# Kernel tuning notes

Hardware: AMD Instinct MI355X
Metric: run time of the kernel (lower is better)

## Reference

```python
import jax, jax.numpy as jnp
import numpy as np

BITS = 8
EPS = 1e-08
D_IN = 4096
D_OUT = 4096


def setup_inputs() -> dict:
    key = jax.random.key(0)
    k1, k2, k3 = jax.random.split(key, 3)
    hidden_states = jax.random.normal(k1, (4, 2048, D_IN), dtype=jnp.float32)
    # Pre-quantized (dequantized-value) weight buffer, as the module stores it in float
    qmax = 2 ** (BITS - 1) - 1
    w = jax.random.normal(k2, (D_IN, D_OUT), dtype=jnp.float32) * 0.02
    w_scale = jnp.max(jnp.abs(w)) / qmax
    weight_quantized = jnp.clip(jnp.round(w / w_scale), -qmax, qmax) * w_scale
    bias = jax.random.normal(k3, (D_OUT,), dtype=jnp.float32) * 0.01
    x_scale = jnp.asarray(3.0, dtype=jnp.float32)  # calibrated activation maxabs
    return {
        "hidden_states": hidden_states,
        "weight_quantized": weight_quantized,
        "x_scale": x_scale,
        "bias": bias,
    }


def _quantize_maxabs(x, scale, bits, eps):
    # scalar max-abs quantization with a fixed (calibrated) scale
    qmax = 2 ** (bits - 1) - 1
    step = jnp.maximum(scale, eps) / qmax
    return jnp.clip(jnp.round(x / step), -qmax, qmax) * step


def reference(hidden_states, weight_quantized, x_scale, bias):
    orig_shape = hidden_states.shape[:-1]
    d = hidden_states.shape[-1]
    x_flat = hidden_states.reshape(-1, d)
    x_q = _quantize_maxabs(x_flat, x_scale, BITS, EPS).astype(weight_quantized.dtype)
    out = x_q @ weight_quantized  # [tokens, d_out]
    out = out + bias.astype(out.dtype)[None, :]
    out = out.astype(hidden_states.dtype)
    return out.reshape(*orig_shape, weight_quantized.shape[1])
```

## Files before the change

kernel.cpp:

```cpp
#include <hip/hip_runtime.h>
#include <hip/hip_bf16.h>
#include <cstdint>

#define D_IN  4096
#define D_OUT 4096

typedef __attribute__((ext_vector_type(4))) int   i32x4;
typedef __attribute__((ext_vector_type(4))) float f32x4;

typedef const __attribute__((address_space(1))) unsigned g_u32;
typedef __attribute__((address_space(3))) unsigned       l_u32;

__global__ void wmax1_kernel(const float* __restrict__ W,
                             float* __restrict__ bmax, int n) {
    __shared__ float red[256];
    int tid = threadIdx.x;
    float m = 0.f;
    for (int i = (blockIdx.x * 256 + tid) * 4; i < n; i += gridDim.x * 256 * 4) {
        float4 v = *(const float4*)(W + i);
        m = fmaxf(m, fmaxf(fmaxf(fabsf(v.x), fabsf(v.y)),
                           fmaxf(fabsf(v.z), fabsf(v.w))));
    }
    red[tid] = m; __syncthreads();
    for (int s = 128; s > 0; s >>= 1) {
        if (tid < s) red[tid] = fmaxf(red[tid], red[tid + s]);
        __syncthreads();
    }
    if (tid == 0) bmax[blockIdx.x] = red[0];
}

__global__ void wmax2_kernel(const float* __restrict__ bmax,
                             float* __restrict__ ws) {
    __shared__ float red[1024];
    int tid = threadIdx.x;
    red[tid] = bmax[tid]; __syncthreads();
    for (int s = 512; s > 0; s >>= 1) {
        if (tid < s) red[tid] = fmaxf(red[tid], red[tid + s]);
        __syncthreads();
    }
    if (tid == 0) ws[0] = red[0] * (1.0f / 127.0f);
}

__global__ void quant_x_kernel(const float* __restrict__ x,
                               char* __restrict__ xq,
                               const float* __restrict__ xscale, int n) {
    int i = (blockIdx.x * blockDim.x + threadIdx.x) * 4;
    if (i >= n) return;
    float inv = 127.0f / fmaxf(xscale[0], 1e-8f);
    float4 v = *(const float4*)(x + i);
    char4 o;
    o.x = (char)fminf(fmaxf(rintf(v.x * inv), -127.f), 127.f);
    o.y = (char)fminf(fmaxf(rintf(v.y * inv), -127.f), 127.f);
    o.z = (char)fminf(fmaxf(rintf(v.z * inv), -127.f), 127.f);
    o.w = (char)fminf(fmaxf(rintf(v.w * inv), -127.f), 127.f);
    *(char4*)(xq + i) = o;
}

__global__ void convW_kernel(const float* __restrict__ W,
                             char* __restrict__ Wt,
                             const float* __restrict__ ws) {
    __shared__ float tile[32][33];
    float invws = 1.0f / ws[0];
    int n0 = blockIdx.x * 32, k0 = blockIdx.y * 32;
    tile[threadIdx.y][threadIdx.x] =
        W[(size_t)(k0 + threadIdx.y) * D_OUT + n0 + threadIdx.x];
    __syncthreads();
    Wt[(size_t)(n0 + threadIdx.y) * D_IN + k0 + threadIdx.x] =
        (char)rintf(tile[threadIdx.x][threadIdx.y] * invws);
}

__global__ __launch_bounds__(512, 2)
void gemm_kernel(const char* __restrict__ A,
                 const char* __restrict__ Bt,
                 const float* __restrict__ bias,
                 const float* __restrict__ xscale,
                 const float* __restrict__ wsp,
                 float* __restrict__ C, int M) {
    constexpr int K = D_IN, N = D_OUT;
    constexpr int NT = K / 128;
    __shared__ char lds[2 * 65536];

    const int tid  = threadIdx.x;
    const int lane = tid & 63;
    const int wid  = tid >> 6;
    const int wr   = wid >> 2;
    const int wc   = wid & 3;

    const int nTn = N / 256;
    const int nwg = gridDim.x;
    int bid = blockIdx.x;
    int q8 = nwg >> 3, r8 = nwg & 7;
    int xcd = bid & 7, idx = bid >> 3;
    int swz = (xcd < r8 ? xcd * (q8 + 1) : r8 * (q8 + 1) + (xcd - r8) * q8) + idx;
    const int tm = swz / nTn, tn = swz % nTn;
    const int row0 = tm * 256, col0 = tn * 256;

    int srcOff[4], dstOff[4];
#pragma unroll
    for (int i = 0; i < 4; ++i) {
        int p  = (i * 512 + tid) * 16;
        int sw = p ^ (((p >> 7) & 7) << 4);
        dstOff[i] = p;
        srcOff[i] = (sw >> 7) * K + (sw & 127);
    }

    const char* srcA = A  + (size_t)row0 * K;
    const char* srcB = Bt + (size_t)col0 * K;
    char* ldsb = lds;

    auto STAGE4 = [&](const char* src, char* dst) {
#pragma unroll
        for (int i = 0; i < 4; ++i)
            __builtin_amdgcn_global_load_lds((g_u32*)(src + srcOff[i]),
                                             (l_u32*)(dst + dstOff[i]), 16, 0, 0);
    };
    auto STAGE2 = [&](const char* src, char* dst) {
#pragma unroll
        for (int i = 0; i < 2; ++i)
            __builtin_amdgcn_global_load_lds((g_u32*)(src + srcOff[i]),
                                             (l_u32*)(dst + dstOff[i]), 16, 0, 0);
    };

    STAGE2(srcB, ldsb + 32768);
    STAGE4(srcA, ldsb);
    STAGE2(srcB + 128 * K, ldsb + 32768 + 16384);
    STAGE2(srcB + 128,     ldsb + 65536 + 32768);
    STAGE4(srcA + 128,     ldsb + 65536);

    i32x4 acc[8][4];
#pragma unroll
    for (int m = 0; m < 8; ++m)
#pragma unroll
        for (int n = 0; n < 4; ++n) acc[m][n] = (i32x4){0, 0, 0, 0};

    const int cp0 = (((lane >> 4) << 4)) ^ ((lane & 7) << 4);
    const int cp1 = cp0 ^ 64;
    const int aBase = (wr * 128 + (lane & 15)) * 128;
    const int bBase = (wc * 64  + (lane & 15)) * 128;

    asm volatile("s_waitcnt vmcnt(6)" ::: "memory");

    auto KITER = [&](int t, char* cur, char* nxt) {
        i32x4 a[4][2], b01[2][2], b23[2][2];
        const char* cA = cur;
        const char* cB = cur + 32768;

        __builtin_amdgcn_s_barrier();
        if (t + 1 < NT) STAGE2(srcB + 128 * K + (t + 1) * 128, nxt + 32768 + 16384);

#pragma unroll
        for (int n = 0; n < 2; ++n) {
            b01[n][0] = *(const i32x4*)(cB + bBase + n * 2048 + cp0);
            b01[n][1] = *(const i32x4*)(cB + bBase + n * 2048 + cp1);
        }
#pragma unroll
        for (int m = 0; m < 4; ++m) {
            a[m][0] = *(const i32x4*)(cA + aBase + m * 2048 + cp0);
            a[m][1] = *(const i32x4*)(cA + aBase + m * 2048 + cp1);
        }
#pragma unroll
        for (int n = 0; n < 2; ++n) {
            b23[n][0] = *(const i32x4*)(cB + bBase + 4096 + n * 2048 + cp0);
            b23[n][1] = *(const i32x4*)(cB + bBase + 4096 + n * 2048 + cp1);
        }

        __builtin_amdgcn_s_setprio(1);
#pragma unroll
        for (int m = 0; m < 4; ++m)
#pragma unroll
            for (int n = 0; n < 2; ++n) {
                acc[m][n] = __builtin_amdgcn_mfma_i32_16x16x64_i8(a[m][0], b01[n][0], acc[m][n], 0, 0, 0);
                acc[m][n] = __builtin_amdgcn_mfma_i32_16x16x64_i8(a[m][1], b01[n][1], acc[m][n], 0, 0, 0);
            }
#pragma unroll
        for (int m = 0; m < 4; ++m)
#pragma unroll
            for (int n = 0; n < 2; ++n) {
                acc[m][n + 2] = __builtin_amdgcn_mfma_i32_16x16x64_i8(a[m][0], b23[n][0], acc[m][n + 2], 0, 0, 0);
                acc[m][n + 2] = __builtin_amdgcn_mfma_i32_16x16x64_i8(a[m][1], b23[n][1], acc[m][n + 2], 0, 0, 0);
            }
#pragma unroll
        for (int m = 0; m < 4; ++m) {
            a[m][0] = *(const i32x4*)(cA + aBase + 8192 + m * 2048 + cp0);
            a[m][1] = *(const i32x4*)(cA + aBase + 8192 + m * 2048 + cp1);
        }
#pragma unroll
        for (int m = 0; m < 4; ++m)
#pragma unroll
            for (int n = 0; n < 2; ++n) {
                acc[m + 4][n + 2] = __builtin_amdgcn_mfma_i32_16x16x64_i8(a[m][0], b23[n][0], acc[m + 4][n + 2], 0, 0, 0);
                acc[m + 4][n + 2] = __builtin_amdgcn_mfma_i32_16x16x64_i8(a[m][1], b23[n][1], acc[m + 4][n + 2], 0, 0, 0);
            }
#pragma unroll
        for (int m = 0; m < 4; ++m)
#pragma unroll
            for (int n = 0; n < 2; ++n) {
                acc[m + 4][n] = __builtin_amdgcn_mfma_i32_16x16x64_i8(a[m][0], b01[n][0], acc[m + 4][n], 0, 0, 0);
                acc[m + 4][n] = __builtin_amdgcn_mfma_i32_16x16x64_i8(a[m][1], b01[n][1], acc[m + 4][n], 0, 0, 0);
            }
        __builtin_amdgcn_s_setprio(0);

        __builtin_amdgcn_s_barrier();
        if (t + 2 < NT) {
            STAGE2(srcB + (t + 2) * 128, cur + 32768);
            STAGE4(srcA + (t + 2) * 128, cur);
            asm volatile("s_waitcnt vmcnt(6)" ::: "memory");
        } else {
            asm volatile("s_waitcnt vmcnt(0)" ::: "memory");
        }
    };

    for (int t = 0; t < NT; t += 2) {
        KITER(t,     ldsb,         ldsb + 65536);
        KITER(t + 1, ldsb + 65536, ldsb);
    }

    const float scale = (fmaxf(xscale[0], 1e-8f) * (1.0f / 127.0f)) * wsp[0];
    const int lr = (lane >> 4) * 4, lc = lane & 15;
#pragma unroll
    for (int n = 0; n < 4; ++n) {
        int col = col0 + wc * 64 + n * 16 + lc;
        float bv = bias[col];
#pragma unroll
        for (int m = 0; m < 8; ++m) {
            int rowb = row0 + wr * 128 + m * 16 + lr;
            i32x4 v = acc[m][n];
#pragma unroll
            for (int r2 = 0; r2 < 4; ++r2)
                C[(size_t)(rowb + r2) * N + col] = (float)v[r2] * scale + bv;
        }
    }
}

extern "C" void kernel_launch(void* const* d_in, const int* in_sizes, int n_in,
                              void* d_out, int out_size, void* d_ws, size_t ws_size,
                              hipStream_t stream) {
    const float* x      = (const float*)d_in[0];
    const float* W      = (const float*)d_in[1];
    const float* xscale = (const float*)d_in[2];
    const float* bias   = (const float*)d_in[3];
    float* out = (float*)d_out;

    const int nx = in_sizes[0];
    const int nw = in_sizes[1];
    const int M  = nx / D_IN;

    char*  xq   = (char*)d_ws;
    char*  Wt   = (char*)d_ws + (size_t)nx;
    float* bmax = (float*)((char*)d_ws + (size_t)nx + nw);
    float* wsp  = bmax + 1024;

    wmax1_kernel<<<1024, 256, 0, stream>>>(W, bmax, nw);
    wmax2_kernel<<<1, 1024, 0, stream>>>(bmax, wsp);

    quant_x_kernel<<<nx / 4 / 256, 256, 0, stream>>>(x, xq, xscale, nx);

    dim3 tb(32, 32);
    dim3 tg(D_OUT / 32, D_IN / 32);
    convW_kernel<<<tg, tb, 0, stream>>>(W, Wt, wsp);

    int grid = (M / 256) * (D_OUT / 256);
    gemm_kernel<<<grid, 512, 0, stream>>>(xq, Wt, bias, xscale, wsp, out, M);
}
```

Baseline: 209.9 us.

## Fuse prep kernels and switch GEMM to 32x32x32 int8 MFMA tiles

Merges the weight max-reduction stage 1 and activation quantization into one launch, and folds the final weight-scale reduction into every convW block, which drops two launches. The GEMM inner loop moves from 16x16x64 to 32x32x32 int8 MFMA with 16-wide accumulators and new swizzled LDS offsets, and the epilogue is rewritten for the 32x32 output layout. In exchange, each of the 16K convW blocks now repeats a 1024-element reduction, and the larger MFMA shape changes register pressure and LDS read patterns.

```diff
diff --git a/kernel.cpp b/kernel.cpp
--- a/kernel.cpp
+++ b/kernel.cpp
@@ -5,62 +5,63 @@
 #define D_IN  4096
 #define D_OUT 4096
 
-typedef __attribute__((ext_vector_type(4))) int   i32x4;
-typedef __attribute__((ext_vector_type(4))) float f32x4;
+typedef __attribute__((ext_vector_type(4)))  int   i32x4;
+typedef __attribute__((ext_vector_type(16))) int   i32x16;
 
 typedef const __attribute__((address_space(1))) unsigned g_u32;
 typedef __attribute__((address_space(3))) unsigned       l_u32;
 
-__global__ void wmax1_kernel(const float* __restrict__ W,
-                             float* __restrict__ bmax, int n) {
-    __shared__ float red[256];
+__global__ void prep_kernel(const float* __restrict__ W, int nw,
+                            const float* __restrict__ x,
+                            char* __restrict__ xq,
+                            const float* __restrict__ xscale, int nx,
+                            float* __restrict__ bmax) {
     int tid = threadIdx.x;
-    float m = 0.f;
-    for (int i = (blockIdx.x * 256 + tid) * 4; i < n; i += gridDim.x * 256 * 4) {
-        float4 v = *(const float4*)(W + i);
-        m = fmaxf(m, fmaxf(fmaxf(fabsf(v.x), fabsf(v.y)),
-                           fmaxf(fabsf(v.z), fabsf(v.w))));
-    }
-    red[tid] = m; __syncthreads();
-    for (int s = 128; s > 0; s >>= 1) {
-        if (tid < s) red[tid] = fmaxf(red[tid], red[tid + s]);
-        __syncthreads();
-    }
-    if (tid == 0) bmax[blockIdx.x] = red[0];
-}
-
-__global__ void wmax2_kernel(const float* __restrict__ bmax,
-                             float* __restrict__ ws) {
-    __shared__ float red[1024];
-    int tid = threadIdx.x;
-    red[tid] = bmax[tid]; __syncthreads();
-    for (int s = 512; s > 0; s >>= 1) {
-        if (tid < s) red[tid] = fmaxf(red[tid], red[tid + s]);
-        __syncthreads();
-    }
-    if (tid == 0) ws[0] = red[0] * (1.0f / 127.0f);
-}
-
-__global__ void quant_x_kernel(const float* __restrict__ x,
-                               char* __restrict__ xq,
-                               const float* __restrict__ xscale, int n) {
-    int i = (blockIdx.x * blockDim.x + threadIdx.x) * 4;
-    if (i >= n) return;
-    float inv = 127.0f / fmaxf(xscale[0], 1e-8f);
-    float4 v = *(const float4*)(x + i);
-    char4 o;
-    o.x = (char)fminf(fmaxf(rintf(v.x * inv), -127.f), 127.f);
-    o.y = (char)fminf(fmaxf(rintf(v.y * inv), -127.f), 127.f);
-    o.z = (char)fminf(fmaxf(rintf(v.z * inv), -127.f), 127.f);
-    o.w = (char)fminf(fmaxf(rintf(v.w * inv), -127.f), 127.f);
-    *(char4*)(xq + i) = o;
+    if (blockIdx.x < 1024) {
+        __shared__ float red[256];
+        float m = 0.f;
+        for (int i = (blockIdx.x * 256 + tid) * 4; i < nw; i += 1024 * 256 * 4) {
+            float4 v = *(const float4*)(W + i);
+            m = fmaxf(m, fmaxf(fmaxf(fabsf(v.x), fabsf(v.y)),
+                               fmaxf(fabsf(v.z), fabsf(v.w))));
+        }
+        red[tid] = m; __syncthreads();
+        for (int s = 128; s > 0; s >>= 1) {
+            if (tid < s) red[tid] = fmaxf(red[tid], red[tid + s]);
+            __syncthreads();
+        }
+        if (tid == 0) bmax[blockIdx.x] = red[0];
+    } else {
+        int i = ((blockIdx.x - 1024) * 256 + tid) * 4;
+        if (i >= nx) return;
+        float inv = 127.0f / fmaxf(xscale[0], 1e-8f);
+        float4 v = *(const float4*)(x + i);
+        char4 o;
+        o.x = (char)fminf(fmaxf(rintf(v.x * inv), -127.f), 127.f);
+        o.y = (char)fminf(fmaxf(rintf(v.y * inv), -127.f), 127.f);
+        o.z = (char)fminf(fmaxf(rintf(v.z * inv), -127.f), 127.f);
+        o.w = (char)fminf(fmaxf(rintf(v.w * inv), -127.f), 127.f);
+        *(char4*)(xq + i) = o;
+    }
 }
 
 __global__ void convW_kernel(const float* __restrict__ W,
                              char* __restrict__ Wt,
-                             const float* __restrict__ ws) {
+                             const float* __restrict__ bmax,
+                             float* __restrict__ wsp) {
     __shared__ float tile[32][33];
-    float invws = 1.0f / ws[0];
+    __shared__ float red[1024];
+    int lt = threadIdx.y * 32 + threadIdx.x;
+    red[lt] = bmax[lt]; __syncthreads();
+    for (int s = 512; s > 0; s >>= 1) {
+        if (lt < s) red[lt] = fmaxf(red[lt], red[lt + s]);
+        __syncthreads();
+    }
+    float wmax = red[0];
+    float invws = 127.0f / wmax;
+    if (lt == 0 && blockIdx.x == 0 && blockIdx.y == 0)
+        wsp[0] = wmax * (1.0f / 127.0f);
+
     int n0 = blockIdx.x * 32, k0 = blockIdx.y * 32;
     tile[threadIdx.y][threadIdx.x] =
         W[(size_t)(k0 + threadIdx.y) * D_OUT + n0 + threadIdx.x];
@@ -127,21 +128,26 @@
     STAGE2(srcB + 128,     ldsb + 65536 + 32768);
     STAGE4(srcA + 128,     ldsb + 65536);
 
-    i32x4 acc[8][4];
-#pragma unroll
-    for (int m = 0; m < 8; ++m)
-#pragma unroll
-        for (int n = 0; n < 4; ++n) acc[m][n] = (i32x4){0, 0, 0, 0};
-
-    const int cp0 = (((lane >> 4) << 4)) ^ ((lane & 7) << 4);
-    const int cp1 = cp0 ^ 64;
-    const int aBase = (wr * 128 + (lane & 15)) * 128;
-    const int bBase = (wc * 64  + (lane & 15)) * 128;
+    i32x16 acc[4][2];
+#pragma unroll
+    for (int m = 0; m < 4; ++m)
+#pragma unroll
+        for (int n = 0; n < 2; ++n)
+#pragma unroll
+            for (int r = 0; r < 16; ++r) acc[m][n][r] = 0;
+
+    const int sw7 = (lane & 7) << 4;
+    const int hi16 = (lane >> 5) * 16;
+    int coff[4];
+#pragma unroll
+    for (int ks = 0; ks < 4; ++ks) coff[ks] = (ks * 32 + hi16) ^ sw7;
+    const int aRow = (wr * 128 + (lane & 31)) * 128;
+    const int bRow = (wc * 64  + (lane & 31)) * 128;
 
     asm volatile("s_waitcnt vmcnt(6)" ::: "memory");
 
     auto KITER = [&](int t, char* cur, char* nxt) {
-        i32x4 a[4][2], b01[2][2], b23[2][2];
+        i32x4 a[4][2], b[2][2];
         const char* cA = cur;
         const char* cB = cur + 32768;
 
@@ -150,53 +156,41 @@
 
 #pragma unroll
         for (int n = 0; n < 2; ++n) {
-            b01[n][0] = *(const i32x4*)(cB + bBase + n * 2048 + cp0);
-            b01[n][1] = *(const i32x4*)(cB + bBase + n * 2048 + cp1);
+            b[n][0] = *(const i32x4*)(cB + bRow + n * 4096 + coff[0]);
+            b[n][1] = *(const i32x4*)(cB + bRow + n * 4096 + coff[1]);
         }
 #pragma unroll
         for (int m = 0; m < 4; ++m) {
-            a[m][0] = *(const i32x4*)(cA + aBase + m * 2048 + cp0);
-            a[m][1] = *(const i32x4*)(cA + aBase + m * 2048 + cp1);
-        }
+            a[m][0] = *(const i32x4*)(cA + aRow + m * 4096 + coff[0]);
+            a[m][1] = *(const i32x4*)(cA + aRow + m * 4096 + coff[1]);
+        }
+        __builtin_amdgcn_s_setprio(1);
+#pragma unroll
+        for (int m = 0; m < 4; ++m)
+#pragma unroll
+            for (int n = 0; n < 2; ++n) {
+                acc[m][n] = __builtin_amdgcn_mfma_i32_32x32x32_i8(a[m][0], b[n][0], acc[m][n], 0, 0, 0);
+                acc[m][n] = __builtin_amdgcn_mfma_i32_32x32x32_i8(a[m][1], b[n][1], acc[m][n], 0, 0, 0);
+            }
+        __builtin_amdgcn_s_setprio(0);
+
 #pragma unroll
         for (int n = 0; n < 2; ++n) {
-            b23[n][0] = *(const i32x4*)(cB + bBase + 4096 + n * 2048 + cp0);
-            b23[n][1] = *(const i32x4*)(cB + bBase + 4096 + n * 2048 + cp1);
-        }
-
+            b[n][0] = *(const i32x4*)(cB + bRow + n * 4096 + coff[2]);
+            b[n][1] = *(const i32x4*)(cB + bRow + n * 4096 + coff[3]);
+        }
+#pragma unroll
+        for (int m = 0; m < 4; ++m) {
+            a[m][0] = *(const i32x4*)(cA + aRow + m * 4096 + coff[2]);
+            a[m][1] = *(const i32x4*)(cA + aRow + m * 4096 + coff[3]);
+        }
         __builtin_amdgcn_s_setprio(1);
 #pragma unroll
         for (int m = 0; m < 4; ++m)
 #pragma unroll
             for (int n = 0; n < 2; ++n) {
-                acc[m][n] = __builtin_amdgcn_mfma_i32_16x16x64_i8(a[m][0], b01[n][0], acc[m][n], 0, 0, 0);
-                acc[m][n] = __builtin_amdgcn_mfma_i32_16x16x64_i8(a[m][1], b01[n][1], acc[m][n], 0, 0, 0);
-            }
-#pragma unroll
-        for (int m = 0; m < 4; ++m)
-#pragma unroll
-            for (int n = 0; n < 2; ++n) {
-                acc[m][n + 2] = __builtin_amdgcn_mfma_i32_16x16x64_i8(a[m][0], b23[n][0], acc[m][n + 2], 0, 0, 0);
-                acc[m][n + 2] = __builtin_amdgcn_mfma_i32_16x16x64_i8(a[m][1], b23[n][1], acc[m][n + 2], 0, 0, 0);
-            }
-#pragma unroll
-        for (int m = 0; m < 4; ++m) {
-            a[m][0] = *(const i32x4*)(cA + aBase + 8192 + m * 2048 + cp0);
-            a[m][1] = *(const i32x4*)(cA + aBase + 8192 + m * 2048 + cp1);
-        }
-#pragma unroll
-        for (int m = 0; m < 4; ++m)
-#pragma unroll
-            for (int n = 0; n < 2; ++n) {
-                acc[m + 4][n + 2] = __builtin_amdgcn_mfma_i32_16x16x64_i8(a[m][0], b23[n][0], acc[m + 4][n + 2], 0, 0, 0);
-                acc[m + 4][n + 2] = __builtin_amdgcn_mfma_i32_16x16x64_i8(a[m][1], b23[n][1], acc[m + 4][n + 2], 0, 0, 0);
-            }
-#pragma unroll
-        for (int m = 0; m < 4; ++m)
-#pragma unroll
-            for (int n = 0; n < 2; ++n) {
-                acc[m + 4][n] = __builtin_amdgcn_mfma_i32_16x16x64_i8(a[m][0], b01[n][0], acc[m + 4][n], 0, 0, 0);
-                acc[m + 4][n] = __builtin_amdgcn_mfma_i32_16x16x64_i8(a[m][1], b01[n][1], acc[m + 4][n], 0, 0, 0);
+                acc[m][n] = __builtin_amdgcn_mfma_i32_32x32x32_i8(a[m][0], b[n][0], acc[m][n], 0, 0, 0);
+                acc[m][n] = __builtin_amdgcn_mfma_i32_32x32x32_i8(a[m][1], b[n][1], acc[m][n], 0, 0, 0);
             }
         __builtin_amdgcn_s_setprio(0);
 
@@ -216,18 +210,20 @@
     }
 
     const float scale = (fmaxf(xscale[0], 1e-8f) * (1.0f / 127.0f)) * wsp[0];
-    const int lr = (lane >> 4) * 4, lc = lane & 15;
-#pragma unroll
-    for (int n = 0; n < 4; ++n) {
-        int col = col0 + wc * 64 + n * 16 + lc;
+    const int lc = lane & 31, lr = 4 * (lane >> 5);
+#pragma unroll
+    for (int n = 0; n < 2; ++n) {
+        int col = col0 + wc * 64 + n * 32 + lc;
         float bv = bias[col];
 #pragma unroll
-        for (int m = 0; m < 8; ++m) {
-            int rowb = row0 + wr * 128 + m * 16 + lr;
-            i32x4 v = acc[m][n];
-#pragma unroll
-            for (int r2 = 0; r2 < 4; ++r2)
-                C[(size_t)(rowb + r2) * N + col] = (float)v[r2] * scale + bv;
+        for (int m = 0; m < 4; ++m) {
+            int rowb = row0 + wr * 128 + m * 32 + lr;
+            i32x16 v = acc[m][n];
+#pragma unroll
+            for (int reg = 0; reg < 16; ++reg) {
+                int r = (reg & 3) + 8 * (reg >> 2);
+                C[(size_t)(rowb + r) * N + col] = (float)v[reg] * scale + bv;
+            }
         }
     }
 }
@@ -250,14 +246,12 @@
     float* bmax = (float*)((char*)d_ws + (size_t)nx + nw);
     float* wsp  = bmax + 1024;
 
-    wmax1_kernel<<<1024, 256, 0, stream>>>(W, bmax, nw);
-    wmax2_kernel<<<1, 1024, 0, stream>>>(bmax, wsp);
-
-    quant_x_kernel<<<nx / 4 / 256, 256, 0, stream>>>(x, xq, xscale, nx);
+    int qblocks = nx / 4 / 256;
+    prep_kernel<<<1024 + qblocks, 256, 0, stream>>>(W, nw, x, xq, xscale, nx, bmax);
 
     dim3 tb(32, 32);
     dim3 tg(D_OUT / 32, D_IN / 32);
-    convW_kernel<<<tg, tb, 0, stream>>>(W, Wt, wsp);
+    convW_kernel<<<tg, tb, 0, stream>>>(W, Wt, bmax, wsp);
 
     int grid = (M / 256) * (D_OUT / 256);
     gemm_kernel<<<grid, 512, 0, stream>>>(xq, Wt, bias, xscale, wsp, out, M);
```

New measurement: 239.9 us. 14.3% more time.

## Restructure int8 GEMM to K=64 tiles with split A/B staging; fuse prep kernels

Applied to the files above, without the earlier changes.

Merges the weight max-abs reduction and activation quantization into one launch to cut a kernel launch. Rewrites the GEMM main loop to use 64-wide K tiles in two 32KB LDS buffers, with a new swizzle. A and B are staged separately and interleaved with two half-tile MFMA phases, using register double-buffering of B fragments. The aim is lower LDS footprint and finer-grained overlap of global-to-LDS copies with MFMA work, at the cost of twice as many loop iterations and more barriers.

```diff
diff --git a/kernel.cpp b/kernel.cpp
--- a/kernel.cpp
+++ b/kernel.cpp
@@ -5,28 +5,43 @@
 #define D_IN  4096
 #define D_OUT 4096
 
-typedef __attribute__((ext_vector_type(4))) int   i32x4;
-typedef __attribute__((ext_vector_type(4))) float f32x4;
+typedef __attribute__((ext_vector_type(4)))  int   i32x4;
 
 typedef const __attribute__((address_space(1))) unsigned g_u32;
 typedef __attribute__((address_space(3))) unsigned       l_u32;
 
-__global__ void wmax1_kernel(const float* __restrict__ W,
-                             float* __restrict__ bmax, int n) {
-    __shared__ float red[256];
+__global__ void prep_kernel(const float* __restrict__ W, int nw,
+                            const float* __restrict__ x,
+                            char* __restrict__ xq,
+                            const float* __restrict__ xscale, int nx,
+                            float* __restrict__ bmax) {
     int tid = threadIdx.x;
-    float m = 0.f;
-    for (int i = (blockIdx.x * 256 + tid) * 4; i < n; i += gridDim.x * 256 * 4) {
-        float4 v = *(const float4*)(W + i);
-        m = fmaxf(m, fmaxf(fmaxf(fabsf(v.x), fabsf(v.y)),
-                           fmaxf(fabsf(v.z), fabsf(v.w))));
-    }
-    red[tid] = m; __syncthreads();
-    for (int s = 128; s > 0; s >>= 1) {
-        if (tid < s) red[tid] = fmaxf(red[tid], red[tid + s]);
-        __syncthreads();
-    }
-    if (tid == 0) bmax[blockIdx.x] = red[0];
+    if (blockIdx.x < 1024) {
+        __shared__ float red[256];
+        float m = 0.f;
+        for (int i = (blockIdx.x * 256 + tid) * 4; i < nw; i += 1024 * 256 * 4) {
+            float4 v = *(const float4*)(W + i);
+            m = fmaxf(m, fmaxf(fmaxf(fabsf(v.x), fabsf(v.y)),
+                               fmaxf(fabsf(v.z), fabsf(v.w))));
+        }
+        red[tid] = m; __syncthreads();
+        for (int s = 128; s > 0; s >>= 1) {
+            if (tid < s) red[tid] = fmaxf(red[tid], red[tid + s]);
+            __syncthreads();
+        }
+        if (tid == 0) bmax[blockIdx.x] = red[0];
+    } else {
+        int i = ((blockIdx.x - 1024) * 256 + tid) * 4;
+        if (i >= nx) return;
+        float inv = 127.0f / fmaxf(xscale[0], 1e-8f);
+        float4 v = *(const float4*)(x + i);
+        char4 o;
+        o.x = (char)fminf(fmaxf(rintf(v.x * inv), -127.f), 127.f);
+        o.y = (char)fminf(fmaxf(rintf(v.y * inv), -127.f), 127.f);
+        o.z = (char)fminf(fmaxf(rintf(v.z * inv), -127.f), 127.f);
+        o.w = (char)fminf(fmaxf(rintf(v.w * inv), -127.f), 127.f);
+        *(char4*)(xq + i) = o;
+    }
 }
 
 __global__ void wmax2_kernel(const float* __restrict__ bmax,
@@ -39,21 +54,6 @@
         __syncthreads();
     }
     if (tid == 0) ws[0] = red[0] * (1.0f / 127.0f);
-}
-
-__global__ void quant_x_kernel(const float* __restrict__ x,
-                               char* __restrict__ xq,
-                               const float* __restrict__ xscale, int n) {
-    int i = (blockIdx.x * blockDim.x + threadIdx.x) * 4;
-    if (i >= n) return;
-    float inv = 127.0f / fmaxf(xscale[0], 1e-8f);
-    float4 v = *(const float4*)(x + i);
-    char4 o;
-    o.x = (char)fminf(fmaxf(rintf(v.x * inv), -127.f), 127.f);
-    o.y = (char)fminf(fmaxf(rintf(v.y * inv), -127.f), 127.f);
-    o.z = (char)fminf(fmaxf(rintf(v.z * inv), -127.f), 127.f);
-    o.w = (char)fminf(fmaxf(rintf(v.w * inv), -127.f), 127.f);
-    *(char4*)(xq + i) = o;
 }
 
 __global__ void convW_kernel(const float* __restrict__ W,
@@ -77,8 +77,8 @@
                  const float* __restrict__ wsp,
                  float* __restrict__ C, int M) {
     constexpr int K = D_IN, N = D_OUT;
-    constexpr int NT = K / 128;
-    __shared__ char lds[2 * 65536];
+    constexpr int NT = K / 64;
+    __shared__ char lds[2 * 32768];
 
     const int tid  = threadIdx.x;
     const int lane = tid & 63;
@@ -95,37 +95,35 @@
     const int tm = swz / nTn, tn = swz % nTn;
     const int row0 = tm * 256, col0 = tn * 256;
 
-    int srcOff[4], dstOff[4];
-#pragma unroll
-    for (int i = 0; i < 4; ++i) {
+    int srcOff[2], dstOff[2];
+#pragma unroll
+    for (int i = 0; i < 2; ++i) {
         int p  = (i * 512 + tid) * 16;
-        int sw = p ^ (((p >> 7) & 7) << 4);
+        int sw = p ^ (((p >> 6) & 3) << 4);
         dstOff[i] = p;
-        srcOff[i] = (sw >> 7) * K + (sw & 127);
+        srcOff[i] = (sw >> 6) * K + (sw & 63);
     }
 
     const char* srcA = A  + (size_t)row0 * K;
     const char* srcB = Bt + (size_t)col0 * K;
-    char* ldsb = lds;
-
-    auto STAGE4 = [&](const char* src, char* dst) {
-#pragma unroll
-        for (int i = 0; i < 4; ++i)
-            __builtin_amdgcn_global_load_lds((g_u32*)(src + srcOff[i]),
-                                             (l_u32*)(dst + dstOff[i]), 16, 0, 0);
+    char* b0 = lds;
+    char* b1 = lds + 32768;
+
+    auto STAGEA = [&](int t, char* buf) {
+#pragma unroll
+        for (int i = 0; i < 2; ++i)
+            __builtin_amdgcn_global_load_lds((g_u32*)(srcA + t * 64 + srcOff[i]),
+                                             (l_u32*)(buf + dstOff[i]), 16, 0, 0);
     };
-    auto STAGE2 = [&](const char* src, char* dst) {
+    auto STAGEB = [&](int t, char* buf) {
 #pragma unroll
         for (int i = 0; i < 2; ++i)
-            __builtin_amdgcn_global_load_lds((g_u32*)(src + srcOff[i]),
-                                             (l_u32*)(dst + dstOff[i]), 16, 0, 0);
+            __builtin_amdgcn_global_load_lds((g_u32*)(srcB + t * 64 + srcOff[i]),
+                                             (l_u32*)(buf + 16384 + dstOff[i]), 16, 0, 0);
     };
 
-    STAGE2(srcB, ldsb + 32768);
-    STAGE4(srcA, ldsb);
-    STAGE2(srcB + 128 * K, ldsb + 32768 + 16384);
-    STAGE2(srcB + 128,     ldsb + 65536 + 32768);
-    STAGE4(srcA + 128,     ldsb + 65536);
+    STAGEA(0, b0); STAGEB(0, b0);
+    STAGEB(1, b1); STAGEA(1, b1);
 
     i32x4 acc[8][4];
 #pragma unroll
@@ -133,86 +131,61 @@
 #pragma unroll
         for (int n = 0; n < 4; ++n) acc[m][n] = (i32x4){0, 0, 0, 0};
 
-    const int cp0 = (((lane >> 4) << 4)) ^ ((lane & 7) << 4);
-    const int cp1 = cp0 ^ 64;
-    const int aBase = (wr * 128 + (lane & 15)) * 128;
-    const int bBase = (wc * 64  + (lane & 15)) * 128;
-
-    asm volatile("s_waitcnt vmcnt(6)" ::: "memory");
-
-    auto KITER = [&](int t, char* cur, char* nxt) {
-        i32x4 a[4][2], b01[2][2], b23[2][2];
-        const char* cA = cur;
-        const char* cB = cur + 32768;
-
-        __builtin_amdgcn_s_barrier();
-        if (t + 1 < NT) STAGE2(srcB + 128 * K + (t + 1) * 128, nxt + 32768 + 16384);
-
-#pragma unroll
-        for (int n = 0; n < 2; ++n) {
-            b01[n][0] = *(const i32x4*)(cB + bBase + n * 2048 + cp0);
-            b01[n][1] = *(const i32x4*)(cB + bBase + n * 2048 + cp1);
-        }
-#pragma unroll
-        for (int m = 0; m < 4; ++m) {
-            a[m][0] = *(const i32x4*)(cA + aBase + m * 2048 + cp0);
-            a[m][1] = *(const i32x4*)(cA + aBase + m * 2048 + cp1);
-        }
-#pragma unroll
-        for (int n = 0; n < 2; ++n) {
-            b23[n][0] = *(const i32x4*)(cB + bBase + 4096 + n * 2048 + cp0);
-            b23[n][1] = *(const i32x4*)(cB + bBase + 4096 + n * 2048 + cp1);
-        }
-
+    const int cOff  = (((lane >> 4) ^ (lane & 3)) << 4);
+    const int aBase = (wr * 128 + (lane & 15)) * 64 + cOff;
+    const int bBase = 16384 + (wc * 64 + (lane & 15)) * 64 + cOff;
+
+    i32x4 aA[4], aB[4], bE[4], bO[4];
+
+    asm volatile("s_waitcnt vmcnt(4)" ::: "memory");
+    __builtin_amdgcn_s_barrier();
+#pragma unroll
+    for (int m = 0; m < 4; ++m) aA[m] = *(const i32x4*)(b0 + aBase + m * 1024);
+#pragma unroll
+    for (int n = 0; n < 4; ++n) bE[n] = *(const i32x4*)(b0 + bBase + n * 1024);
+    asm volatile("s_waitcnt lgkmcnt(0)" ::: "memory");
+    __builtin_amdgcn_s_barrier();
+
+    auto KTILE = [&](int t, char* cur, char* nxt, i32x4* bUse, i32x4* bLoad) {
+#pragma unroll
+        for (int m = 0; m < 4; ++m) aB[m] = *(const i32x4*)(cur + aBase + 4096 + m * 1024);
+        bool st = (t + 2 < NT);
+        if (st) STAGEB(t + 2, cur);
+        __builtin_amdgcn_s_barrier();
+        asm volatile("s_waitcnt lgkmcnt(0)" ::: "memory");
         __builtin_amdgcn_s_setprio(1);
 #pragma unroll
         for (int m = 0; m < 4; ++m)
 #pragma unroll
-            for (int n = 0; n < 2; ++n) {
-                acc[m][n] = __builtin_amdgcn_mfma_i32_16x16x64_i8(a[m][0], b01[n][0], acc[m][n], 0, 0, 0);
-                acc[m][n] = __builtin_amdgcn_mfma_i32_16x16x64_i8(a[m][1], b01[n][1], acc[m][n], 0, 0, 0);
-            }
+            for (int n = 0; n < 4; ++n)
+                acc[m][n] = __builtin_amdgcn_mfma_i32_16x16x64_i8(aA[m], bUse[n], acc[m][n], 0, 0, 0);
+        __builtin_amdgcn_s_setprio(0);
+        if (st) { asm volatile("s_waitcnt vmcnt(2)" ::: "memory"); }
+        else    { asm volatile("s_waitcnt vmcnt(0)" ::: "memory"); }
+        __builtin_amdgcn_s_barrier();
+
+        if (t + 1 < NT) {
+#pragma unroll
+            for (int m = 0; m < 4; ++m) aA[m] = *(const i32x4*)(nxt + aBase + m * 1024);
+#pragma unroll
+            for (int n = 0; n < 4; ++n) bLoad[n] = *(const i32x4*)(nxt + bBase + n * 1024);
+        }
+        if (st) STAGEA(t + 2, cur);
+        __builtin_amdgcn_s_barrier();
+        asm volatile("s_waitcnt lgkmcnt(0)" ::: "memory");
+        __builtin_amdgcn_s_setprio(1);
 #pragma unroll
         for (int m = 0; m < 4; ++m)
 #pragma unroll
-            for (int n = 0; n < 2; ++n) {
-                acc[m][n + 2] = __builtin_amdgcn_mfma_i32_16x16x64_i8(a[m][0], b23[n][0], acc[m][n + 2], 0, 0, 0);
-                acc[m][n + 2] = __builtin_amdgcn_mfma_i32_16x16x64_i8(a[m][1], b23[n][1], acc[m][n + 2], 0, 0, 0);
-            }
-#pragma unroll
-        for (int m = 0; m < 4; ++m) {
-            a[m][0] = *(const i32x4*)(cA + aBase + 8192 + m * 2048 + cp0);
-            a[m][1] = *(const i32x4*)(cA + aBase + 8192 + m * 2048 + cp1);
-        }
-#pragma unroll
-        for (int m = 0; m < 4; ++m)
-#pragma unroll
-            for (int n = 0; n < 2; ++n) {
-                acc[m + 4][n + 2] = __builtin_amdgcn_mfma_i32_16x16x64_i8(a[m][0], b23[n][0], acc[m + 4][n + 2], 0, 0, 0);
-                acc[m + 4][n + 2] = __builtin_amdgcn_mfma_i32_16x16x64_i8(a[m][1], b23[n][1], acc[m + 4][n + 2], 0, 0, 0);
-            }
-#pragma unroll
-        for (int m = 0; m < 4; ++m)
-#pragma unroll
-            for (int n = 0; n < 2; ++n) {
-                acc[m + 4][n] = __builtin_amdgcn_mfma_i32_16x16x64_i8(a[m][0], b01[n][0], acc[m + 4][n], 0, 0, 0);
-                acc[m + 4][n] = __builtin_amdgcn_mfma_i32_16x16x64_i8(a[m][1], b01[n][1], acc[m + 4][n], 0, 0, 0);
-            }
+            for (int n = 0; n < 4; ++n)
+                acc[m + 4][n] = __builtin_amdgcn_mfma_i32_16x16x64_i8(aB[m], bUse[n], acc[m + 4][n], 0, 0, 0);
         __builtin_amdgcn_s_setprio(0);
-
-        __builtin_amdgcn_s_barrier();
-        if (t + 2 < NT) {
-            STAGE2(srcB + (t + 2) * 128, cur + 32768);
-            STAGE4(srcA + (t + 2) * 128, cur);
-            asm volatile("s_waitcnt vmcnt(6)" ::: "memory");
-        } else {
-            asm volatile("s_waitcnt vmcnt(0)" ::: "memory");
-        }
+        __builtin_amdgcn_s_barrier();
     };
 
     for (int t = 0; t < NT; t += 2) {
-        KITER(t,     ldsb,         ldsb + 65536);
-        KITER(t + 1, ldsb + 65536, ldsb);
+        KTILE(t,     b0, b1, bE, bO);
+        KTILE(t + 1, b1, b0, bO, bE);
     }
 
     const float scale = (fmaxf(xscale[0], 1e-8f) * (1.0f / 127.0f)) * wsp[0];
@@ -250,10 +223,9 @@
     float* bmax = (float*)((char*)d_ws + (size_t)nx + nw);
     float* wsp  = bmax + 1024;
 
-    wmax1_kernel<<<1024, 256, 0, stream>>>(W, bmax, nw);
+    int qblocks = nx / 4 / 256;
+    prep_kernel<<<1024 + qblocks, 256, 0, stream>>>(W, nw, x, xq, xscale, nx, bmax);
     wmax2_kernel<<<1, 1024, 0, stream>>>(bmax, wsp);
-
-    quant_x_kernel<<<nx / 4 / 256, 256, 0, stream>>>(x, xq, xscale, nx);
 
     dim3 tb(32, 32);
     dim3 tg(D_OUT / 32, D_IN / 32);
```

New measurement: 216.0 us. +2.9%, slower.
